# Kernel optimization log

Measured on AMD Instinct MI355X. Metric: run time of the kernel, lower is better.

## Reference

```python
import jax, jax.numpy as jnp
import numpy as np

N = 32768   # total nodes
E = 524288  # total edges (avg degree 16)
D = 128     # dim_h == input_size
H = 4       # attention heads
B = 64      # graphs per batch
S = 512     # nodes per graph (N = B*S, equal-size graphs)
EPS = 1e-5


def _lin(key, out_d, in_d):
    kw, kb = jax.random.split(key)
    s = 1.0 / np.sqrt(in_d)
    W = jax.random.uniform(kw, (out_d, in_d), minval=-s, maxval=s, dtype=jnp.float32)
    b = jax.random.uniform(kb, (out_d,), minval=-s, maxval=s, dtype=jnp.float32)
    return W, b


def setup_inputs() -> dict:
    key = jax.random.key(0)
    ks = jax.random.split(key, 16)
    x = jax.random.normal(ks[0], (N, D), dtype=jnp.float32)
    edge_index = jax.random.randint(ks[1], (2, E), 0, N, dtype=jnp.int64)
    batch_ids = (jnp.arange(N) // S).astype(jnp.int64)
    Wres, bres = _lin(ks[2], D, D)          # res_lin (MLPStack([in, dim_h]))
    Wk, bk = _lin(ks[3], D, D)              # ResGatedGraphConv lin_key
    Wq, bq = _lin(ks[4], D, D)              # lin_query
    Wv, bv = _lin(ks[5], D, D)              # lin_value
    Wskip, bskip = _lin(ks[6], D, D)        # lin_skip
    in_proj_w, in_proj_b = _lin(ks[7], 3 * D, D)   # MHA in_proj
    out_proj_w, out_proj_b = _lin(ks[8], D, D)     # MHA out_proj
    W1, b1 = _lin(ks[9], 2 * D, D)          # ff_linear1
    W2, b2 = _lin(ks[10], D, 2 * D)         # ff_linear2
    g1l = jax.random.normal(ks[11], (D,), dtype=jnp.float32) * 0.1 + 1.0
    b1l = jax.random.normal(ks[12], (D,), dtype=jnp.float32) * 0.1
    g1a = jax.random.normal(ks[13], (D,), dtype=jnp.float32) * 0.1 + 1.0
    b1a = jax.random.normal(ks[14], (D,), dtype=jnp.float32) * 0.1
    kg, kb2 = jax.random.split(ks[15])
    g2 = jax.random.normal(kg, (D,), dtype=jnp.float32) * 0.1 + 1.0
    b2g = jax.random.normal(kb2, (D,), dtype=jnp.float32) * 0.1
    return dict(x=x, edge_index=edge_index, batch_ids=batch_ids,
                Wres=Wres, bres=bres, Wk=Wk, bk=bk, Wq=Wq, bq=bq, Wv=Wv, bv=bv,
                Wskip=Wskip, bskip=bskip, g1l=g1l, b1l=b1l, g1a=g1a, b1a=b1a,
                in_proj_w=in_proj_w, in_proj_b=in_proj_b,
                out_proj_w=out_proj_w, out_proj_b=out_proj_b,
                W1=W1, b1=b1, W2=W2, b2=b2, g2=g2, b2g=b2g)


def _bn(h, g, b):
    # BatchNorm1d in eval mode, running_mean=0, running_var=1
    return h * (g / jnp.sqrt(1.0 + EPS)) + b


def _forward(x, edge_index, Wres, bres, Wk, bk, Wq, bq, Wv, bv, Wskip, bskip,
             g1l, b1l, g1a, b1a, in_proj_w, in_proj_b, out_proj_w, out_proj_b,
             W1, b1, W2, b2, g2, b2g):
    src, dst = edge_index[0], edge_index[1]
    # residual projection (MLPStack([input_size, dim_h]) -> Linear + ReLU)
    h_in1 = jax.nn.relu(x @ Wres.T + bres)

    # --- local: ResGatedGraphConv ---
    k = x @ Wk.T + bk   # keyed by target node
    q = x @ Wq.T + bq   # queried by source node
    v = x @ Wv.T + bv
    msg = jax.nn.sigmoid(k[dst] + q[src]) * v[src]                 # [E, D]
    agg = jax.ops.segment_sum(msg, dst, num_segments=N)            # [N, D]
    h_local = agg + (x @ Wskip.T + bskip)
    h_local = _bn(h_in1 + h_local, g1l, b1l)

    # --- global: dense-batch multihead attention (equal graphs, no padding) ---
    hd = D // H
    h_dense = h_in1.reshape(B, S, D)
    qkv = h_dense @ in_proj_w.T + in_proj_b                        # [B, S, 3D]
    qh, kh, vh = jnp.split(qkv, 3, axis=-1)
    qh = qh.reshape(B, S, H, hd)
    kh = kh.reshape(B, S, H, hd)
    vh = vh.reshape(B, S, H, hd)
    scores = jnp.einsum('bqhd,bkhd->bhqk', qh, kh) / np.sqrt(hd)   # [B, H, S, S]
    attn = jax.nn.softmax(scores, axis=-1)
    ctx = jnp.einsum('bhqk,bkhd->bqhd', attn, vh).reshape(B, S, D)
    h_attn = (ctx @ out_proj_w.T + out_proj_b).reshape(N, D)
    h_attn = _bn(h_in1 + h_attn, g1a, b1a)

    # --- combine + FFN ---
    h = h_local + h_attn
    ff = jax.nn.relu(h @ W1.T + b1) @ W2.T + b2
    h = _bn(h + ff, g2, b2g)
    return h


def reference(x, edge_index, batch_ids, Wres, bres, Wk, bk, Wq, bq, Wv, bv,
              Wskip, bskip, g1l, b1l, g1a, b1a, in_proj_w, in_proj_b,
              out_proj_w, out_proj_b, W1, b1, W2, b2, g2, b2g):
    return _forward(x, edge_index, Wres, bres, Wk, bk, Wq, bq, Wv, bv,
                    Wskip, bskip, g1l, b1l, g1a, b1a, in_proj_w, in_proj_b,
                    out_proj_w, out_proj_b, W1, b1, W2, b2, g2, b2g)
```

## Files before the change

kernel.cpp:

```cpp
#include <hip/hip_runtime.h>
#include <math.h>

#define N_NODES 32768
#define N_EDGES 524288
#define DIM     128
#define CAP     80

static constexpr size_t NM = (size_t)N_NODES * DIM;

typedef __attribute__((ext_vector_type(8)))  short bf8;
typedef __attribute__((ext_vector_type(4)))  float f32x4;
typedef __attribute__((ext_vector_type(16))) float f32x16;

__device__ __forceinline__ short f2bs(float x) {
    union { float f; unsigned int u; } v; v.f = x;
    unsigned int r = v.u + 0x7fffu + ((v.u >> 16) & 1u);
    return (short)(r >> 16);
}
__device__ __forceinline__ unsigned int pk2(float a, float b) {
    return (unsigned int)(unsigned short)f2bs(a) |
           ((unsigned int)(unsigned short)f2bs(b) << 16);
}
__device__ __forceinline__ float2 bs2f(unsigned int u) {
    union { unsigned int a; float f; } lo, hi;
    lo.a = u << 16; hi.a = u & 0xffff0000u;
    float2 r; r.x = lo.f; r.y = hi.f; return r;
}
__device__ __forceinline__ float bs1f(short s) {
    union { unsigned int a; float f; } t;
    t.a = ((unsigned int)(unsigned short)s) << 16; return t.f;
}

__global__ __launch_bounds__(256)
void cvt_scatter_kernel(const float* __restrict__ x,
                        const float* __restrict__ w0, const float* __restrict__ w1,
                        const float* __restrict__ w2, const float* __restrict__ w3,
                        const float* __restrict__ w4, const float* __restrict__ w5,
                        const float* __restrict__ w6, const float* __restrict__ w7,
                        const float* __restrict__ w8,
                        const float* __restrict__ b0, const float* __restrict__ b1,
                        const float* __restrict__ b2, const float* __restrict__ b3,
                        const float* __restrict__ b4,
                        const int* __restrict__ ei,
                        short* __restrict__ xb, short* __restrict__ wbf,
                        float* __restrict__ bcat,
                        int* __restrict__ deg, unsigned short* __restrict__ slots)
{
    if (blockIdx.x < 2048) {
        int e = blockIdx.x * 256 + threadIdx.x;
        int d = ei[N_EDGES + e];
        int pos = atomicAdd(&deg[d], 1);
        if (pos < CAP) slots[d * CAP + pos] = (unsigned short)ei[e];
        return;
    }
    long long t = (long long)(blockIdx.x - 2048) * 256 + threadIdx.x;
    long long i4 = t * 4;
    if (i4 < (long long)NM) {
        float4 v = *(const float4*)(x + i4);
        short4 o; o.x = f2bs(v.x); o.y = f2bs(v.y); o.z = f2bs(v.z); o.w = f2bs(v.w);
        *(short4*)(xb + i4) = o;
    } else {
        int j = (int)(i4 - (long long)NM);
        if (j < 212992) {
            const float* src; int off;
            if      (j <  16384) { src = w0; off = 0; }
            else if (j <  32768) { src = w1; off = 16384; }
            else if (j <  49152) { src = w2; off = 32768; }
            else if (j <  65536) { src = w3; off = 49152; }
            else if (j <  81920) { src = w4; off = 65536; }
            else if (j < 131072) { src = w5; off = 81920; }
            else if (j < 147456) { src = w6; off = 131072; }
            else if (j < 180224) { src = w7; off = 147456; }
            else                 { src = w8; off = 180224; }
            float4 v = *(const float4*)(src + (j - off));
            short4 o; o.x = f2bs(v.x); o.y = f2bs(v.y); o.z = f2bs(v.z); o.w = f2bs(v.w);
            *(short4*)(wbf + j) = o;
        } else if (j < 213632) {
            int jb = j - 212992;
            int grp = jb >> 7, loc = jb & 127;
            const float* bs = (grp == 0) ? b0 : (grp == 1) ? b1 :
                              (grp == 2) ? b2 : (grp == 3) ? b3 : b4;
            float4 v = *(const float4*)(bs + loc);
            *(float4*)(bcat + jb) = v;
        }
    }
}

__global__ __launch_bounds__(256)
void proj5_kernel(const short* __restrict__ xb, const short* __restrict__ wbf,
                  const float* __restrict__ bcat,
                  short* __restrict__ hin1b, short* __restrict__ kbv,
                  short* __restrict__ qvb, short* __restrict__ skipb)
{
    const int g  = blockIdx.x / 512;
    const int my = blockIdx.x % 512;
    const int lane = threadIdx.x & 63;
    const int wid  = threadIdx.x >> 6;
    const int m0 = my * 64 + (wid >> 1) * 32;
    const int n0 = (wid & 1) * 64;
    const int lrow = lane & 15;
    const int lk   = (lane >> 4) * 8;

    f32x4 acc[2][4] = {};
    const short* Ap = xb + (size_t)(m0 + lrow) * 128 + lk;
    const short* Wp = wbf + g * 16384 + (size_t)(n0 + lrow) * 128 + lk;
    #pragma unroll
    for (int ks = 0; ks < 128; ks += 32) {
        bf8 af[2], wf[4];
        af[0] = *(const bf8*)(Ap + ks);
        af[1] = *(const bf8*)(Ap + 16 * 128 + ks);
        #pragma unroll
        for (int j = 0; j < 4; ++j) wf[j] = *(const bf8*)(Wp + (size_t)j * 16 * 128 + ks);
        #pragma unroll
        for (int i = 0; i < 2; ++i)
            #pragma unroll
            for (int j = 0; j < 4; ++j)
                acc[i][j] = __builtin_amdgcn_mfma_f32_16x16x32_bf16(af[i], wf[j], acc[i][j], 0, 0, 0);
    }
    const int rbase = (lane >> 4) * 4;
    #pragma unroll
    for (int j = 0; j < 4; ++j) {
        int col = n0 + j * 16 + lrow;
        float bcol = bcat[g * 128 + col];
        #pragma unroll
        for (int i = 0; i < 2; ++i)
            #pragma unroll
            for (int r = 0; r < 4; ++r) {
                int row = m0 + i * 16 + rbase + r;
                float v = acc[i][j][r] + bcol;
                if (g == 0)      { v = fmaxf(v, 0.f); hin1b[(size_t)row * 128 + col] = f2bs(v); }
                else if (g == 1) kbv[(size_t)row * 128 + col] = f2bs(v);
                else if (g == 2) qvb[(size_t)row * 256 + col * 2] = f2bs(v);
                else if (g == 3) qvb[(size_t)row * 256 + col * 2 + 1] = f2bs(v);
                else             skipb[(size_t)row * 128 + col] = f2bs(v);
            }
    }
}

__global__ __launch_bounds__(256)
void inproj_kernel(const short* __restrict__ hin1b, const short* __restrict__ wbf,
                   const float* __restrict__ bin, short* __restrict__ qkvb,
                   float qscale)
{
    const int gx = blockIdx.x % 3;
    const int my = blockIdx.x / 3;
    const int lane = threadIdx.x & 63;
    const int wid  = threadIdx.x >> 6;
    const int m0 = my * 64 + (wid >> 1) * 32;
    const int n0 = (wid & 1) * 64;
    const int lrow = lane & 15;
    const int lk   = (lane >> 4) * 8;

    f32x4 acc[2][4] = {};
    const short* Ap = hin1b + (size_t)(m0 + lrow) * 128 + lk;
    const short* Wp = wbf + 81920 + (size_t)(gx * 128 + n0 + lrow) * 128 + lk;
    #pragma unroll
    for (int ks = 0; ks < 128; ks += 32) {
        bf8 af[2], wf[4];
        af[0] = *(const bf8*)(Ap + ks);
        af[1] = *(const bf8*)(Ap + 16 * 128 + ks);
        #pragma unroll
        for (int j = 0; j < 4; ++j) wf[j] = *(const bf8*)(Wp + (size_t)j * 16 * 128 + ks);
        #pragma unroll
        for (int i = 0; i < 2; ++i)
            #pragma unroll
            for (int j = 0; j < 4; ++j)
                acc[i][j] = __builtin_amdgcn_mfma_f32_16x16x32_bf16(af[i], wf[j], acc[i][j], 0, 0, 0);
    }
    const int rbase = (lane >> 4) * 4;
    #pragma unroll
    for (int j = 0; j < 4; ++j) {
        int col = gx * 128 + n0 + j * 16 + lrow;
        float bcol = bin[col];
        float sc = (col < 128) ? qscale : 1.0f;
        #pragma unroll
        for (int i = 0; i < 2; ++i)
            #pragma unroll
            for (int r = 0; r < 4; ++r) {
                int row = m0 + i * 16 + rbase + r;
                float v = (acc[i][j][r] + bcol) * sc;
                qkvb[(size_t)row * 384 + col] = f2bs(v);
            }
    }
}

__global__ __launch_bounds__(256)
void gather_local_kernel(const unsigned int* __restrict__ kbu,
                         const uint2* __restrict__ qvu,
                         const unsigned int* __restrict__ skipu,
                         const unsigned int* __restrict__ hin1u,
                         const int* __restrict__ deg,
                         const unsigned short* __restrict__ slots,
                         const float* __restrict__ g, const float* __restrict__ beta,
                         unsigned int* __restrict__ hlocal_u)
{
    const int d    = blockIdx.x * 4 + (threadIdx.x >> 6);
    const int lane = threadIdx.x & 63;
    const float rs = 0.9999950000374998f;

    float2 k2 = bs2f(kbu[(size_t)d * 64 + lane]);
    int dg = deg[d]; if (dg > CAP) dg = CAP;
    const unsigned short* sp = slots + (size_t)d * CAP;
    int i = 0;

    float ax = 0.f, ay = 0.f, cx = 0.f, cy = 0.f;
    for (; i + 8 <= dg; i += 8) {
        int s[8];
        #pragma unroll
        for (int u = 0; u < 8; ++u) s[u] = sp[i + u];
        uint2 w[8];
        #pragma unroll
        for (int u = 0; u < 8; ++u) w[u] = qvu[(size_t)s[u] * 64 + lane];
        #pragma unroll
        for (int u = 0; u < 8; ++u) {
            float2 pa = bs2f(w[u].x), pb = bs2f(w[u].y);
            if (u & 1) {
                cx += pa.y * __builtin_amdgcn_rcpf(1.0f + __expf(-(k2.x + pa.x)));
                cy += pb.y * __builtin_amdgcn_rcpf(1.0f + __expf(-(k2.y + pb.x)));
            } else {
                ax += pa.y * __builtin_amdgcn_rcpf(1.0f + __expf(-(k2.x + pa.x)));
                ay += pb.y * __builtin_amdgcn_rcpf(1.0f + __expf(-(k2.y + pb.x)));
            }
        }
    }
    for (; i + 4 <= dg; i += 4) {
        int s0 = sp[i], s1 = sp[i + 1], s2 = sp[i + 2], s3 = sp[i + 3];
        uint2 w0 = qvu[(size_t)s0 * 64 + lane];
        uint2 w1 = qvu[(size_t)s1 * 64 + lane];
        uint2 w2 = qvu[(size_t)s2 * 64 + lane];
        uint2 w3 = qvu[(size_t)s3 * 64 + lane];
        float2 p0 = bs2f(w0.x), p1 = bs2f(w0.y);
        float2 p2 = bs2f(w1.x), p3 = bs2f(w1.y);
        float2 p4 = bs2f(w2.x), p5 = bs2f(w2.y);
        float2 p6 = bs2f(w3.x), p7 = bs2f(w3.y);
        ax += p0.y * __builtin_amdgcn_rcpf(1.0f + __expf(-(k2.x + p0.x)));
        ay += p1.y * __builtin_amdgcn_rcpf(1.0f + __expf(-(k2.y + p1.x)));
        cx += p2.y * __builtin_amdgcn_rcpf(1.0f + __expf(-(k2.x + p2.x)));
        cy += p3.y * __builtin_amdgcn_rcpf(1.0f + __expf(-(k2.y + p3.x)));
        ax += p4.y * __builtin_amdgcn_rcpf(1.0f + __expf(-(k2.x + p4.x)));
        ay += p5.y * __builtin_amdgcn_rcpf(1.0f + __expf(-(k2.y + p5.x)));
        cx += p6.y * __builtin_amdgcn_rcpf(1.0f + __expf(-(k2.x + p6.x)));
        cy += p7.y * __builtin_amdgcn_rcpf(1.0f + __expf(-(k2.y + p7.x)));
    }
    for (; i < dg; ++i) {
        int s0 = sp[i];
        uint2 w0 = qvu[(size_t)s0 * 64 + lane];
        float2 p0 = bs2f(w0.x), p1 = bs2f(w0.y);
        ax += p0.y * __builtin_amdgcn_rcpf(1.0f + __expf(-(k2.x + p0.x)));
        ay += p1.y * __builtin_amdgcn_rcpf(1.0f + __expf(-(k2.y + p1.x)));
    }
    ax += cx; ay += cy;

    float2 sk = bs2f(skipu[(size_t)d * 64 + lane]);
    float2 hi = bs2f(hin1u[(size_t)d * 64 + lane]);
    float2 gv = *(const float2*)(g + lane * 2);
    float2 bt = *(const float2*)(beta + lane * 2);
    float ox = (hi.x + sk.x + ax) * (gv.x * rs) + bt.x;
    float oy = (hi.y + sk.y + ay) * (gv.y * rs) + bt.y;
    hlocal_u[(size_t)d * 64 + lane] = pk2(ox, oy);
}

__device__ __forceinline__ void lswap(unsigned int& X, unsigned int& Y, bool hi) {
    unsigned int Xs = (unsigned int)__shfl_xor((int)X, 32);
    unsigned int Ys = (unsigned int)__shfl_xor((int)Y, 32);
    unsigned int Xn = hi ? Ys : X;
    unsigned int Yn = hi ? Y  : Xs;
    X = Xn; Y = Yn;
}

__global__ __launch_bounds__(512)
void attn_mfma(const short* __restrict__ qkv, short* __restrict__ ctx)
{
    __shared__ __align__(16) short ldsK[512 * 40];
    __shared__ __align__(16) short ldsVt[32 * 512];

    const int blk  = blockIdx.x;
    const int h    = blk & 3;
    const int b    = blk >> 2;
    const int tid  = threadIdx.x;
    const int lane = tid & 63;
    const int wid  = tid >> 6;
    const int lq = lane & 31;
    const int lg = lane >> 5;
    const size_t gbase = (size_t)(b * 512) * 384 + h * 32;

    #pragma unroll
    for (int i = 0; i < 4; ++i) {
        int c = tid + i * 512;
        int key = c >> 2, part = c & 3;
        bf8 v = *(const bf8*)(qkv + gbase + (size_t)key * 384 + 128 + part * 8);
        *(bf8*)(ldsK + key * 40 + part * 8) = v;
    }
    if (tid < 256) {
        int p = tid;
        const short* v0 = qkv + gbase + (size_t)(2 * p) * 384 + 256;
        const short* v1 = v0 + 384;
        bf8 r0[4], r1[4];
        #pragma unroll
        for (int i = 0; i < 4; ++i) { r0[i] = *(const bf8*)(v0 + i * 8);
                                      r1[i] = *(const bf8*)(v1 + i * 8); }
        #pragma unroll
        for (int d = 0; d < 32; ++d) {
            unsigned int w = ((unsigned int)(unsigned short)r0[d >> 3][d & 7]) |
                             (((unsigned int)(unsigned short)r1[d >> 3][d & 7]) << 16);
            *(unsigned int*)((char*)ldsVt + d * 1024 + ((4 * p) ^ ((d & 7) << 4))) = w;
        }
    }
    const int qoff = wid * 64;
    bf8 qf[2][2];
    #pragma unroll
    for (int qg = 0; qg < 2; ++qg)
        #pragma unroll
        for (int kh = 0; kh < 2; ++kh)
            qf[qg][kh] = *(const bf8*)(qkv + gbase +
                           (size_t)(qoff + qg * 32 + lq) * 384 + kh * 16 + lg * 8);
    __syncthreads();

    const f32x16 Z16 = {0.f,0.f,0.f,0.f,0.f,0.f,0.f,0.f,0.f,0.f,0.f,0.f,0.f,0.f,0.f,0.f};
    f32x16 o[2] = {Z16, Z16};
    float mreg[2] = {-1e30f, -1e30f};
    float lreg[2] = {0.f, 0.f};
    const bool hiw = (lg != 0);

    for (int kt = 0; kt < 16; ++kt) {
        bf8 ak[2], vt[2];
        #pragma unroll
        for (int kh = 0; kh < 2; ++kh) {
            ak[kh] = *(const bf8*)(ldsK + (kt * 32 + lq) * 40 + kh * 16 + lg * 8);
            int kbyte = (kt * 32 + kh * 16 + lg * 8) * 2;
            vt[kh] = *(const bf8*)((const char*)ldsVt + lq * 1024 +
                                   (kbyte ^ ((lq & 7) << 4)));
        }
        #pragma unroll
        for (int qg = 0; qg < 2; ++qg) {
            f32x16 s = Z16;
            s = __builtin_amdgcn_mfma_f32_32x32x16_bf16(ak[0], qf[qg][0], s, 0, 0, 0);
            s = __builtin_amdgcn_mfma_f32_32x32x16_bf16(ak[1], qf[qg][1], s, 0, 0, 0);
            float t0 = fmaxf(fmaxf(s[0],  s[1]),  s[2]);
            float t1 = fmaxf(fmaxf(s[3],  s[4]),  s[5]);
            float t2 = fmaxf(fmaxf(s[6],  s[7]),  s[8]);
            float t3 = fmaxf(fmaxf(s[9],  s[10]), s[11]);
            float t4 = fmaxf(fmaxf(s[12], s[13]), s[14]);
            float mt = fmaxf(fmaxf(fmaxf(t0, t1), t2), fmaxf(fmaxf(t3, t4), s[15]));
            mt = fmaxf(mt, __shfl_xor(mt, 32));
            if (__any(mt > mreg[qg] + 11.5415603f)) {
                float mnew = fmaxf(mreg[qg], mt);
                float corr = exp2f(mreg[qg] - mnew);
                mreg[qg] = mnew;
                lreg[qg] *= corr;
                #pragma unroll
                for (int r = 0; r < 16; ++r) o[qg][r] *= corr;
            }
            float m = mreg[qg];
            float p[16]; float ps = 0.f;
            #pragma unroll
            for (int r = 0; r < 16; ++r) { p[r] = exp2f(s[r] - m); ps += p[r]; }
            ps += __shfl_xor(ps, 32);
            lreg[qg] += ps;
            unsigned int w0 = pk2(p[0],  p[1]),  w1 = pk2(p[2],  p[3]);
            unsigned int w2 = pk2(p[4],  p[5]),  w3 = pk2(p[6],  p[7]);
            unsigned int w4 = pk2(p[8],  p[9]),  w5 = pk2(p[10], p[11]);
            unsigned int w6 = pk2(p[12], p[13]), w7 = pk2(p[14], p[15]);
            lswap(w0, w2, hiw); lswap(w1, w3, hiw);
            lswap(w4, w6, hiw); lswap(w5, w7, hiw);
            union { unsigned int u[4]; bf8 v; } P0, P1;
            P0.u[0] = w0; P0.u[1] = w1; P0.u[2] = w2; P0.u[3] = w3;
            P1.u[0] = w4; P1.u[1] = w5; P1.u[2] = w6; P1.u[3] = w7;
            o[qg] = __builtin_amdgcn_mfma_f32_32x32x16_bf16(vt[0], P0.v, o[qg], 0, 0, 0);
            o[qg] = __builtin_amdgcn_mfma_f32_32x32x16_bf16(vt[1], P1.v, o[qg], 0, 0, 0);
        }
    }

    __syncthreads();
    short* ldsO = ldsK;
    #pragma unroll
    for (int qg = 0; qg < 2; ++qg) {
        float inv = 1.0f / lreg[qg];
        int ql = qoff + qg * 32 + lq;
        #pragma unroll
        for (int b4 = 0; b4 < 4; ++b4) {
            short4 pkv;
            pkv.x = f2bs(o[qg][b4 * 4 + 0] * inv);
            pkv.y = f2bs(o[qg][b4 * 4 + 1] * inv);
            pkv.z = f2bs(o[qg][b4 * 4 + 2] * inv);
            pkv.w = f2bs(o[qg][b4 * 4 + 3] * inv);
            int dbyte = (8 * b4 + 4 * lg) * 2;
            *(short4*)((char*)ldsO + ql * 64 + (dbyte ^ ((ql & 7) << 3))) = pkv;
        }
    }
    __syncthreads();
    {
        int ql = tid;
        short* dst = ctx + (size_t)(b * 512 + ql) * 128 + h * 32;
        #pragma unroll
        for (int i = 0; i < 8; ++i) {
            short4 part = *(short4*)((char*)ldsO + ql * 64 + ((i * 8) ^ ((ql & 7) << 3)));
            *(short4*)(dst + i * 4) = part;
        }
    }
}

__global__ __launch_bounds__(256)
void outproj_ff_kernel(const short* __restrict__ ctxb, const short* __restrict__ wbf,
                       const float* __restrict__ bout,
                       const short* __restrict__ hin1b, const short* __restrict__ hlocb,
                       const float* __restrict__ g1a, const float* __restrict__ b1a,
                       const float* __restrict__ b1, const float* __restrict__ b2,
                       const float* __restrict__ g2, const float* __restrict__ b2g,
                       float* __restrict__ out)
{
    __shared__ __align__(16) short ldsH[64 * 128];
    __shared__ __align__(16) short ldsF[64 * 256];
    const int my = blockIdx.x;
    const int lane = threadIdx.x & 63;
    const int wid  = threadIdx.x >> 6;
    const int lrow = lane & 15;
    const int lk   = (lane >> 4) * 8;
    const int rbase = (lane >> 4) * 4;
    const float rs = 0.9999950000374998f;

    {
        const int m0 = (wid >> 1) * 32;
        const int n0 = (wid & 1) * 64;
        f32x4 acc[2][4] = {};
        const short* Ap = ctxb + (size_t)(my * 64 + m0 + lrow) * 128 + lk;
        const short* Wp = wbf + 131072 + (size_t)(n0 + lrow) * 128 + lk;
        #pragma unroll
        for (int ks = 0; ks < 128; ks += 32) {
            bf8 af[2], wf[4];
            af[0] = *(const bf8*)(Ap + ks);
            af[1] = *(const bf8*)(Ap + 16 * 128 + ks);
            #pragma unroll
            for (int j = 0; j < 4; ++j) wf[j] = *(const bf8*)(Wp + (size_t)j * 16 * 128 + ks);
            #pragma unroll
            for (int i = 0; i < 2; ++i)
                #pragma unroll
                for (int j = 0; j < 4; ++j)
                    acc[i][j] = __builtin_amdgcn_mfma_f32_16x16x32_bf16(af[i], wf[j], acc[i][j], 0, 0, 0);
        }
        #pragma unroll
        for (int j = 0; j < 4; ++j) {
            int col = n0 + j * 16 + lrow;
            float bcol = bout[col];
            float gsc = g1a[col] * rs;
            float bsc = b1a[col];
            #pragma unroll
            for (int i = 0; i < 2; ++i)
                #pragma unroll
                for (int r = 0; r < 4; ++r) {
                    int rl = m0 + i * 16 + rbase + r;
                    size_t idx = (size_t)(my * 64 + rl) * 128 + col;
                    float v = acc[i][j][r] + bcol;
                    float o = bs1f(hlocb[idx]) + (bs1f(hin1b[idx]) + v) * gsc + bsc;
                    int byte = (rl * 256 + col * 2) ^ ((rl & 7) << 4);
                    *(short*)((char*)ldsH + byte) = f2bs(o);
                }
        }
    }
    __syncthreads();
    {
        const int m0 = (wid >> 1) * 32;
        const int n0 = (wid & 1) * 128;
        f32x4 acc[2][8] = {};
        const short* Wp = wbf + 147456 + (size_t)(n0 + lrow) * 128 + lk;
        #pragma unroll
        for (int ks = 0; ks < 128; ks += 32) {
            bf8 af[2], wf[8];
            #pragma unroll
            for (int i = 0; i < 2; ++i) {
                int row = m0 + lrow + i * 16;
                int byte = (row * 256 + (ks + lk) * 2) ^ ((row & 7) << 4);
                af[i] = *(const bf8*)((const char*)ldsH + byte);
            }
            #pragma unroll
            for (int j = 0; j < 8; ++j) wf[j] = *(const bf8*)(Wp + (size_t)j * 16 * 128 + ks);
            #pragma unroll
            for (int i = 0; i < 2; ++i)
                #pragma unroll
                for (int j = 0; j < 8; ++j)
                    acc[i][j] = __builtin_amdgcn_mfma_f32_16x16x32_bf16(af[i], wf[j], acc[i][j], 0, 0, 0);
        }
        #pragma unroll
        for (int j = 0; j < 8; ++j) {
            int col = n0 + j * 16 + lrow;
            float bc = b1[col];
            #pragma unroll
            for (int i = 0; i < 2; ++i)
                #pragma unroll
                for (int r = 0; r < 4; ++r) {
                    int rl = m0 + i * 16 + rbase + r;
                    float v = fmaxf(acc[i][j][r] + bc, 0.f);
                    int byte = (rl * 512 + col * 2) ^ ((rl & 7) << 4);
                    *(short*)((char*)ldsF + byte) = f2bs(v);
                }
        }
    }
    __syncthreads();
    {
        const int m0 = (wid >> 1) * 32;
        const int n0 = (wid & 1) * 64;
        f32x4 acc[2][4] = {};
        const short* Wp = wbf + 180224 + (size_t)(n0 + lrow) * 256 + lk;
        #pragma unroll
        for (int ks = 0; ks < 256; ks += 32) {
            bf8 af[2], wf[4];
            #pragma unroll
            for (int i = 0; i < 2; ++i) {
                int row = m0 + lrow + i * 16;
                int byte = (row * 512 + (ks + lk) * 2) ^ ((row & 7) << 4);
                af[i] = *(const bf8*)((const char*)ldsF + byte);
            }
            #pragma unroll
            for (int j = 0; j < 4; ++j) wf[j] = *(const bf8*)(Wp + (size_t)j * 16 * 256 + ks);
            #pragma unroll
            for (int i = 0; i < 2; ++i)
                #pragma unroll
                for (int j = 0; j < 4; ++j)
                    acc[i][j] = __builtin_amdgcn_mfma_f32_16x16x32_bf16(af[i], wf[j], acc[i][j], 0, 0, 0);
        }
        #pragma unroll
        for (int j = 0; j < 4; ++j) {
            int col = n0 + j * 16 + lrow;
            float bc = b2[col];
            float gsc = g2[col] * rs;
            float bsc = b2g[col];
            #pragma unroll
            for (int i = 0; i < 2; ++i)
                #pragma unroll
                for (int r = 0; r < 4; ++r) {
                    int rl = m0 + i * 16 + rbase + r;
                    int hbyte = (rl * 256 + col * 2) ^ ((rl & 7) << 4);
                    float hres = bs1f(*(const short*)((const char*)ldsH + hbyte));
                    float v = acc[i][j][r] + bc;
                    out[(size_t)(my * 64 + rl) * 128 + col] = (hres + v) * gsc + bsc;
                }
        }
    }
}

extern "C" void kernel_launch(void* const* d_in, const int* in_sizes, int n_in,
                              void* d_out, int out_size, void* d_ws, size_t ws_size,
                              hipStream_t stream)
{
    (void)in_sizes; (void)n_in; (void)out_size; (void)ws_size;

    const float* x    = (const float*)d_in[0];
    const int*   ei   = (const int*)d_in[1];
    const float* Wres = (const float*)d_in[3];
    const float* bres = (const float*)d_in[4];
    const float* Wk   = (const float*)d_in[5];
    const float* bk   = (const float*)d_in[6];
    const float* Wq   = (const float*)d_in[7];
    const float* bq   = (const float*)d_in[8];
    const float* Wv   = (const float*)d_in[9];
    const float* bv   = (const float*)d_in[10];
    const float* Wsk  = (const float*)d_in[11];
    const float* bsk  = (const float*)d_in[12];
    const float* g1l  = (const float*)d_in[13];
    const float* b1l  = (const float*)d_in[14];
    const float* g1a  = (const float*)d_in[15];
    const float* b1a  = (const float*)d_in[16];
    const float* Win  = (const float*)d_in[17];
    const float* bin  = (const float*)d_in[18];
    const float* Wout = (const float*)d_in[19];
    const float* bout = (const float*)d_in[20];
    const float* W1   = (const float*)d_in[21];
    const float* b1   = (const float*)d_in[22];
    const float* W2   = (const float*)d_in[23];
    const float* b2   = (const float*)d_in[24];
    const float* g2   = (const float*)d_in[25];
    const float* b2g  = (const float*)d_in[26];
    float* out = (float*)d_out;

    float* ws = (float*)d_ws;
    short* hin1b = (short*)ws;
    short* kbv   = (short*)(ws + NM / 2);
    short* qvb   = (short*)(ws + NM);
    short* skipb = (short*)(ws + 2 * NM);
    short* xb    = (short*)(ws + 2 * NM + NM / 2);
    short* qkvb  = (short*)(ws + 3 * NM);
    short* hlocb = (short*)(ws + 4 * NM + NM / 2);
    int* deg = (int*)(ws + 5 * NM);
    unsigned short* slots = (unsigned short*)(deg + N_NODES);
    short* ctxb  = (short*)(ws + 5 * NM);
    short* wbf   = (short*)(ws + 6 * NM);
    float* bcat  = ws + 6 * NM + 106496;

    dim3 blk(256);
    const float qscale = 0.17677669529663687f * 1.4426950408889634f;

    hipMemsetAsync((void*)deg, 0, N_NODES * sizeof(int), stream);

    cvt_scatter_kernel<<<dim3(6353), blk, 0, stream>>>(
        x, Wres, Wk, Wq, Wv, Wsk, Win, Wout, W1, W2,
        bres, bk, bq, bv, bsk, ei, xb, wbf, bcat, deg, slots);

    proj5_kernel<<<dim3(2560), blk, 0, stream>>>(
        xb, wbf, bcat, hin1b, kbv, qvb, skipb);

    inproj_kernel<<<dim3(1536), blk, 0, stream>>>(
        hin1b, wbf, bin, qkvb, qscale);

    gather_local_kernel<<<dim3(N_NODES / 4), blk, 0, stream>>>(
        (const unsigned int*)kbv, (const uint2*)qvb, (const unsigned int*)skipb,
        (const unsigned int*)hin1b, deg, slots, g1l, b1l,
        (unsigned int*)hlocb);

    attn_mfma<<<dim3(256), dim3(512), 0, stream>>>(qkvb, ctxb);

    outproj_ff_kernel<<<dim3(512), blk, 0, stream>>>(
        ctxb, wbf, bout, hin1b, hlocb, g1a, b1a, b1, b2, g2, b2g, out);
}
```

Baseline: 205.3 us.

## Double-buffer K/V staging in attention kernel to overlap loads with MFMA

The attention kernel now stages K and transposed V in four 128-key chunks through two LDS buffers instead of loading all 512 keys before computing. The next chunk's global loads are issued before computing on the current chunk and written to LDS afterward, so memory latency overlaps the MFMA and softmax work. LDS use drops from about 73KB to 36KB, which may allow more blocks per CU. In exchange it adds three extra barriers and some register pressure from holding the prefetched data.

```diff
diff --git a/kernel.cpp b/kernel.cpp
--- a/kernel.cpp
+++ b/kernel.cpp
@@ -271,8 +271,7 @@
 __global__ __launch_bounds__(512)
 void attn_mfma(const short* __restrict__ qkv, short* __restrict__ ctx)
 {
-    __shared__ __align__(16) short ldsK[512 * 40];
-    __shared__ __align__(16) short ldsVt[32 * 512];
+    __shared__ __align__(16) char lds[36864];
 
     const int blk  = blockIdx.x;
     const int h    = blk & 3;
@@ -284,28 +283,39 @@
     const int lg = lane >> 5;
     const size_t gbase = (size_t)(b * 512) * 384 + h * 32;
 
-    #pragma unroll
-    for (int i = 0; i < 4; ++i) {
-        int c = tid + i * 512;
-        int key = c >> 2, part = c & 3;
-        bf8 v = *(const bf8*)(qkv + gbase + (size_t)key * 384 + 128 + part * 8);
-        *(bf8*)(ldsK + key * 40 + part * 8) = v;
-    }
-    if (tid < 256) {
-        int p = tid;
-        const short* v0 = qkv + gbase + (size_t)(2 * p) * 384 + 256;
-        const short* v1 = v0 + 384;
-        bf8 r0[4], r1[4];
-        #pragma unroll
-        for (int i = 0; i < 4; ++i) { r0[i] = *(const bf8*)(v0 + i * 8);
-                                      r1[i] = *(const bf8*)(v1 + i * 8); }
-        #pragma unroll
-        for (int d = 0; d < 32; ++d) {
-            unsigned int w = ((unsigned int)(unsigned short)r0[d >> 3][d & 7]) |
-                             (((unsigned int)(unsigned short)r1[d >> 3][d & 7]) << 16);
-            *(unsigned int*)((char*)ldsVt + d * 1024 + ((4 * p) ^ ((d & 7) << 4))) = w;
-        }
-    }
+    const int skey  = tid >> 2;
+    const int spart = tid & 3;
+    const int vp    = tid & 63;
+    const int vdq   = tid >> 6;
+
+    bf8    kst;
+    short4 v0s, v1s;
+
+    #define STAGE_LOAD(ck)                                                     \
+        kst = *(const bf8*)(qkv + gbase +                                      \
+                (size_t)((ck) * 128 + skey) * 384 + 128 + spart * 8);          \
+        {                                                                      \
+            const short* vr = qkv + gbase +                                    \
+                (size_t)((ck) * 128 + 2 * vp) * 384 + 256 + vdq * 4;           \
+            v0s = *(const short4*)(vr);                                        \
+            v1s = *(const short4*)(vr + 384);                                  \
+        }
+
+    #define STAGE_WRITE(s)                                                     \
+        *(bf8*)((short*)(lds + (s) * 10240) + skey * 40 + spart * 8) = kst;    \
+        {                                                                      \
+            char* vb = lds + 20480 + (s) * 8192;                               \
+            short v0a[4] = {v0s.x, v0s.y, v0s.z, v0s.w};                       \
+            short v1a[4] = {v1s.x, v1s.y, v1s.z, v1s.w};                       \
+            _Pragma("unroll")                                                  \
+            for (int j = 0; j < 4; ++j) {                                      \
+                int d = vdq * 4 + j;                                           \
+                unsigned int w = (unsigned int)(unsigned short)v0a[j] |        \
+                                 ((unsigned int)(unsigned short)v1a[j] << 16); \
+                *(unsigned int*)(vb + d * 256 + ((4 * vp) ^ ((d & 7) << 4))) = w; \
+            }                                                                  \
+        }
+
     const int qoff = wid * 64;
     bf8 qf[2][2];
     #pragma unroll
@@ -314,7 +324,6 @@
         for (int kh = 0; kh < 2; ++kh)
             qf[qg][kh] = *(const bf8*)(qkv + gbase +
                            (size_t)(qoff + qg * 32 + lq) * 384 + kh * 16 + lg * 8);
-    __syncthreads();
 
     const f32x16 Z16 = {0.f,0.f,0.f,0.f,0.f,0.f,0.f,0.f,0.f,0.f,0.f,0.f,0.f,0.f,0.f,0.f};
     f32x16 o[2] = {Z16, Z16};
@@ -322,57 +331,69 @@
     float lreg[2] = {0.f, 0.f};
     const bool hiw = (lg != 0);
 
-    for (int kt = 0; kt < 16; ++kt) {
-        bf8 ak[2], vt[2];
-        #pragma unroll
-        for (int kh = 0; kh < 2; ++kh) {
-            ak[kh] = *(const bf8*)(ldsK + (kt * 32 + lq) * 40 + kh * 16 + lg * 8);
-            int kbyte = (kt * 32 + kh * 16 + lg * 8) * 2;
-            vt[kh] = *(const bf8*)((const char*)ldsVt + lq * 1024 +
-                                   (kbyte ^ ((lq & 7) << 4)));
-        }
-        #pragma unroll
-        for (int qg = 0; qg < 2; ++qg) {
-            f32x16 s = Z16;
-            s = __builtin_amdgcn_mfma_f32_32x32x16_bf16(ak[0], qf[qg][0], s, 0, 0, 0);
-            s = __builtin_amdgcn_mfma_f32_32x32x16_bf16(ak[1], qf[qg][1], s, 0, 0, 0);
-            float t0 = fmaxf(fmaxf(s[0],  s[1]),  s[2]);
-            float t1 = fmaxf(fmaxf(s[3],  s[4]),  s[5]);
-            float t2 = fmaxf(fmaxf(s[6],  s[7]),  s[8]);
-            float t3 = fmaxf(fmaxf(s[9],  s[10]), s[11]);
-            float t4 = fmaxf(fmaxf(s[12], s[13]), s[14]);
-            float mt = fmaxf(fmaxf(fmaxf(t0, t1), t2), fmaxf(fmaxf(t3, t4), s[15]));
-            mt = fmaxf(mt, __shfl_xor(mt, 32));
-            if (__any(mt > mreg[qg] + 11.5415603f)) {
-                float mnew = fmaxf(mreg[qg], mt);
-                float corr = exp2f(mreg[qg] - mnew);
-                mreg[qg] = mnew;
-                lreg[qg] *= corr;
+    STAGE_LOAD(0);
+    STAGE_WRITE(0);
+    __syncthreads();
+
+    for (int c = 0; c < 4; ++c) {
+        if (c < 3) { STAGE_LOAD(c + 1); }
+        const short* Kb = (const short*)(lds + (c & 1) * 10240);
+        const char*  Vb = lds + 20480 + (c & 1) * 8192;
+
+        #pragma unroll
+        for (int ktl = 0; ktl < 4; ++ktl) {
+            bf8 ak[2], vt[2];
+            #pragma unroll
+            for (int kh = 0; kh < 2; ++kh) {
+                ak[kh] = *(const bf8*)(Kb + (ktl * 32 + lq) * 40 + kh * 16 + lg * 8);
+                int kbyte = (ktl * 32 + kh * 16 + lg * 8) * 2;
+                vt[kh] = *(const bf8*)(Vb + lq * 256 + (kbyte ^ ((lq & 7) << 4)));
+            }
+            #pragma unroll
+            for (int qg = 0; qg < 2; ++qg) {
+                f32x16 s = Z16;
+                s = __builtin_amdgcn_mfma_f32_32x32x16_bf16(ak[0], qf[qg][0], s, 0, 0, 0);
+                s = __builtin_amdgcn_mfma_f32_32x32x16_bf16(ak[1], qf[qg][1], s, 0, 0, 0);
+                float t0 = fmaxf(fmaxf(s[0],  s[1]),  s[2]);
+                float t1 = fmaxf(fmaxf(s[3],  s[4]),  s[5]);
+                float t2 = fmaxf(fmaxf(s[6],  s[7]),  s[8]);
+                float t3 = fmaxf(fmaxf(s[9],  s[10]), s[11]);
+                float t4 = fmaxf(fmaxf(s[12], s[13]), s[14]);
+                float mt = fmaxf(fmaxf(fmaxf(t0, t1), t2), fmaxf(fmaxf(t3, t4), s[15]));
+                mt = fmaxf(mt, __shfl_xor(mt, 32));
+                if (__any(mt > mreg[qg] + 11.5415603f)) {
+                    float mnew = fmaxf(mreg[qg], mt);
+                    float corr = exp2f(mreg[qg] - mnew);
+                    mreg[qg] = mnew;
+                    lreg[qg] *= corr;
+                    #pragma unroll
+                    for (int r = 0; r < 16; ++r) o[qg][r] *= corr;
+                }
+                float m = mreg[qg];
+                float p[16]; float ps = 0.f;
                 #pragma unroll
-                for (int r = 0; r < 16; ++r) o[qg][r] *= corr;
+                for (int r = 0; r < 16; ++r) { p[r] = exp2f(s[r] - m); ps += p[r]; }
+                ps += __shfl_xor(ps, 32);
+                lreg[qg] += ps;
+                unsigned int w0 = pk2(p[0],  p[1]),  w1 = pk2(p[2],  p[3]);
+                unsigned int w2 = pk2(p[4],  p[5]),  w3 = pk2(p[6],  p[7]);
+                unsigned int w4 = pk2(p[8],  p[9]),  w5 = pk2(p[10], p[11]);
+                unsigned int w6 = pk2(p[12], p[13]), w7 = pk2(p[14], p[15]);
+                lswap(w0, w2, hiw); lswap(w1, w3, hiw);
+                lswap(w4, w6, hiw); lswap(w5, w7, hiw);
+                union { unsigned int u[4]; bf8 v; } P0, P1;
+                P0.u[0] = w0; P0.u[1] = w1; P0.u[2] = w2; P0.u[3] = w3;
+                P1.u[0] = w4; P1.u[1] = w5; P1.u[2] = w6; P1.u[3] = w7;
+                o[qg] = __builtin_amdgcn_mfma_f32_32x32x16_bf16(vt[0], P0.v, o[qg], 0, 0, 0);
+                o[qg] = __builtin_amdgcn_mfma_f32_32x32x16_bf16(vt[1], P1.v, o[qg], 0, 0, 0);
             }
-            float m = mreg[qg];
-            float p[16]; float ps = 0.f;
-            #pragma unroll
-            for (int r = 0; r < 16; ++r) { p[r] = exp2f(s[r] - m); ps += p[r]; }
-            ps += __shfl_xor(ps, 32);
-            lreg[qg] += ps;
-            unsigned int w0 = pk2(p[0],  p[1]),  w1 = pk2(p[2],  p[3]);
-            unsigned int w2 = pk2(p[4],  p[5]),  w3 = pk2(p[6],  p[7]);
-            unsigned int w4 = pk2(p[8],  p[9]),  w5 = pk2(p[10], p[11]);
-            unsigned int w6 = pk2(p[12], p[13]), w7 = pk2(p[14], p[15]);
-            lswap(w0, w2, hiw); lswap(w1, w3, hiw);
-            lswap(w4, w6, hiw); lswap(w5, w7, hiw);
-            union { unsigned int u[4]; bf8 v; } P0, P1;
-            P0.u[0] = w0; P0.u[1] = w1; P0.u[2] = w2; P0.u[3] = w3;
-            P1.u[0] = w4; P1.u[1] = w5; P1.u[2] = w6; P1.u[3] = w7;
-            o[qg] = __builtin_amdgcn_mfma_f32_32x32x16_bf16(vt[0], P0.v, o[qg], 0, 0, 0);
-            o[qg] = __builtin_amdgcn_mfma_f32_32x32x16_bf16(vt[1], P1.v, o[qg], 0, 0, 0);
-        }
-    }
-
-    __syncthreads();
-    short* ldsO = ldsK;
+        }
+        if (c < 3) { STAGE_WRITE((c + 1) & 1); }
+        __syncthreads();
+    }
+    #undef STAGE_LOAD
+    #undef STAGE_WRITE
+
     #pragma unroll
     for (int qg = 0; qg < 2; ++qg) {
         float inv = 1.0f / lreg[qg];
@@ -385,7 +406,7 @@
             pkv.z = f2bs(o[qg][b4 * 4 + 2] * inv);
             pkv.w = f2bs(o[qg][b4 * 4 + 3] * inv);
             int dbyte = (8 * b4 + 4 * lg) * 2;
-            *(short4*)((char*)ldsO + ql * 64 + (dbyte ^ ((ql & 7) << 3))) = pkv;
+            *(short4*)(lds + ql * 64 + (dbyte ^ ((ql & 7) << 3))) = pkv;
         }
     }
     __syncthreads();
@@ -394,7 +415,7 @@
         short* dst = ctx + (size_t)(b * 512 + ql) * 128 + h * 32;
         #pragma unroll
         for (int i = 0; i < 8; ++i) {
-            short4 part = *(short4*)((char*)ldsO + ql * 64 + ((i * 8) ^ ((ql & 7) << 3)));
+            short4 part = *(short4*)(lds + ql * 64 + ((i * 8) ^ ((ql & 7) << 3)));
             *(short4*)(dst + i * 4) = part;
         }
     }
```

After: 205.7 us. Within noise of the previous version (+0.2%).
